# Kernel tuning notes

Hardware: AMD Instinct MI355X
Metric: run time of the kernel (lower is better)

The kernel has to match this reference:

```python
import jax, jax.numpy as jnp
import numpy as np

N_NODES = 100000
N_EDGES = 1600000
D_IN = 264
D_HID = 64
NEG_SLOPE = 0.2


def _glorot(key, shape):
    fan_in, fan_out = shape[0], shape[-1]
    lim = jnp.sqrt(6.0 / (fan_in + fan_out))
    return jax.random.uniform(key, shape, jnp.float32, -lim, lim)


def setup_inputs() -> dict:
    key = jax.random.key(0)
    ks = jax.random.split(key, 24)
    x = jax.random.normal(ks[0], (N_NODES, D_IN), jnp.float32)
    src = jax.random.randint(ks[1], (N_EDGES,), 0, N_NODES, jnp.int32)
    off = jax.random.randint(ks[2], (N_EDGES,), 1, N_NODES, jnp.int32)
    dst = (src + off) % N_NODES  # guaranteed no self loops
    edge_index = jnp.stack([src, dst], axis=0)
    edge_attr = jax.random.normal(ks[3], (N_EDGES, 1), jnp.float32)
    p = {
        'l1_Wl': _glorot(ks[4], (D_IN, D_HID)), 'l1_bl': jnp.zeros((D_HID,), jnp.float32),
        'l1_Wr': _glorot(ks[5], (D_IN, D_HID)), 'l1_br': jnp.zeros((D_HID,), jnp.float32),
        'l1_We': _glorot(ks[6], (1, D_HID)),
        'l1_att': _glorot(ks[7], (1, 1, D_HID)), 'l1_bias': jnp.zeros((D_HID,), jnp.float32),
        'l2_Wl': _glorot(ks[8], (D_HID, D_HID)), 'l2_bl': jnp.zeros((D_HID,), jnp.float32),
        'l2_Wr': _glorot(ks[9], (D_HID, D_HID)), 'l2_br': jnp.zeros((D_HID,), jnp.float32),
        'l2_We': _glorot(ks[10], (1, D_HID)),
        'l2_att': _glorot(ks[11], (1, 1, D_HID)), 'l2_bias': jnp.zeros((D_HID,), jnp.float32),
        'W3': _glorot(ks[12], (D_HID, D_HID)), 'b3': jnp.zeros((D_HID,), jnp.float32),
        'W4': _glorot(ks[13], (D_HID, 1)), 'b4': jnp.zeros((1,), jnp.float32),
    }
    return dict(x=x, edge_index=edge_index, edge_attr=edge_attr, **p)


def _gatv2_layer(x, src, dst, ea, Wl, bl, Wr, br, We, att, bias):
    # heads=1, concat=True, aggr='max' (passed via **kwargs to MessagePassing)
    n = x.shape[0]
    xl = (x @ Wl + bl).reshape(n, 1, D_HID)  # source-side transform
    xr = (x @ Wr + br).reshape(n, 1, D_HID)  # target-side transform
    e = (ea @ We).reshape(-1, 1, D_HID)      # lin_edge, no bias
    m = jax.nn.leaky_relu(xr[dst] + xl[src] + e, NEG_SLOPE)  # (Etot,1,64)
    logits = jnp.sum(m * att, axis=-1)       # (Etot,1)
    # segment softmax over destination nodes
    mx = jax.ops.segment_max(logits, dst, num_segments=n)
    ex = jnp.exp(logits - mx[dst])
    den = jax.ops.segment_sum(ex, dst, num_segments=n)
    alpha = ex / den[dst]                    # (Etot,1)
    msg = xl[src] * alpha[:, :, None]        # (Etot,1,64)
    out = jax.ops.segment_max(msg, dst, num_segments=n)  # aggr='max'
    return out.reshape(n, D_HID) + bias


def _gcn_forward(x, src, dst, edge_attr,
                 l1_Wl, l1_bl, l1_Wr, l1_br, l1_We, l1_att, l1_bias,
                 l2_Wl, l2_bl, l2_Wr, l2_br, l2_We, l2_att, l2_bias,
                 W3, b3, W4, b4):
    n = x.shape[0]
    # add_self_loops with fill_value='mean' (edges contain no self loops)
    loop = jnp.arange(n, dtype=src.dtype)
    src2 = jnp.concatenate([src, loop])
    dst2 = jnp.concatenate([dst, loop])
    mean_ea = jnp.mean(edge_attr, axis=0, keepdims=True)  # (1,1)
    ea2 = jnp.concatenate([edge_attr, jnp.broadcast_to(mean_ea, (n, 1))], axis=0)
    h = _gatv2_layer(x, src2, dst2, ea2, l1_Wl, l1_bl, l1_Wr, l1_br, l1_We, l1_att, l1_bias)
    h = jax.nn.relu(h)  # dropout inactive in eval
    h = _gatv2_layer(h, src2, dst2, ea2, l2_Wl, l2_bl, l2_Wr, l2_br, l2_We, l2_att, l2_bias)
    h = jax.nn.relu(h)
    h = jax.nn.relu(h @ W3 + b3)
    h = h @ W4 + b4
    return jnp.squeeze(h, axis=-1)  # (N,)


def reference(x, edge_index, edge_attr,
              l1_Wl, l1_bl, l1_Wr, l1_br, l1_We, l1_att, l1_bias,
              l2_Wl, l2_bl, l2_Wr, l2_br, l2_We, l2_att, l2_bias,
              W3, b3, W4, b4):
    src, dst = edge_index[0], edge_index[1]
    return _gcn_forward(x, src, dst, edge_attr,
                        l1_Wl, l1_bl, l1_Wr, l1_br, l1_We, l1_att, l1_bias,
                        l2_Wl, l2_bl, l2_Wr, l2_br, l2_We, l2_att, l2_bias,
                        W3, b3, W4, b4)
```

## Files before the change

kernel.cpp:

```cpp
#include <hip/hip_runtime.h>
#include <math.h>
#include <float.h>

#define NN 100000
#define NE 1600000
#define ETOT 1700000
#define DIN 264
#define DH 64
#define SLOPE 0.2f
#define NB 98

__global__ void k_mean(const float* __restrict__ ea, float* __restrict__ sum) {
  float acc = 0.f;
  for (int i = blockIdx.x * blockDim.x + threadIdx.x; i < NE; i += gridDim.x * blockDim.x)
    acc += ea[i];
  #pragma unroll
  for (int off = 32; off > 0; off >>= 1) acc += __shfl_xor(acc, off);
  __shared__ float s[4];
  int lane = threadIdx.x & 63, w = threadIdx.x >> 6;
  if (lane == 0) s[w] = acc;
  __syncthreads();
  if (threadIdx.x == 0) atomicAdd(sum, s[0] + s[1] + s[2] + s[3]);
}

__global__ void k_hist(const int* __restrict__ ei, unsigned* __restrict__ deg) {
  int e = blockIdx.x * blockDim.x + threadIdx.x;
  if (e >= ETOT) return;
  int d = (e < NE) ? ei[NE + e] : e - NE;
  atomicAdd(&deg[d], 1u);
}


__global__ __launch_bounds__(256)
void k_bsum(const unsigned* __restrict__ deg, unsigned* __restrict__ bsum) {
  int i0 = blockIdx.x * 1024 + threadIdx.x * 4;
  unsigned s = 0;
  if (i0 + 3 < NN) {
    uint4 v = *(const uint4*)&deg[i0];
    s = v.x + v.y + v.z + v.w;
  }
  #pragma unroll
  for (int off = 32; off > 0; off >>= 1) s += __shfl_xor(s, off);
  __shared__ unsigned ws[4];
  int lane = threadIdx.x & 63, w = threadIdx.x >> 6;
  if (lane == 0) ws[w] = s;
  __syncthreads();
  if (threadIdx.x == 0) bsum[blockIdx.x] = ws[0] + ws[1] + ws[2] + ws[3];
}

__global__ __launch_bounds__(128)
void k_sscan(unsigned* __restrict__ bsum, unsigned* __restrict__ rowptr) {
  __shared__ unsigned ls[128];
  int t = threadIdx.x;
  unsigned v = (t < NB) ? bsum[t] : 0u;
  ls[t] = v;
  __syncthreads();
  for (int off = 1; off < 128; off <<= 1) {
    unsigned u = (t >= off) ? ls[t - off] : 0u;
    __syncthreads();
    ls[t] += u;
    __syncthreads();
  }
  if (t < NB) bsum[t] = ls[t] - v;
  if (t == 127) rowptr[NN] = ls[127];
}

__global__ __launch_bounds__(256)
void k_scan2(const unsigned* __restrict__ deg, const unsigned* __restrict__ bsum,
             unsigned* __restrict__ rowptr, unsigned* __restrict__ wptr) {
  __shared__ unsigned ls[256];
  int i0 = blockIdx.x * 1024 + threadIdx.x * 4;
  unsigned d0 = 0, d1 = 0, d2 = 0, d3 = 0;
  if (i0 + 3 < NN) {
    uint4 v = *(const uint4*)&deg[i0];
    d0 = v.x; d1 = v.y; d2 = v.z; d3 = v.w;
  }
  unsigned ts = d0 + d1 + d2 + d3;
  ls[threadIdx.x] = ts;
  __syncthreads();
  for (int off = 1; off < 256; off <<= 1) {
    unsigned u = (threadIdx.x >= (unsigned)off) ? ls[threadIdx.x - off] : 0u;
    __syncthreads();
    ls[threadIdx.x] += u;
    __syncthreads();
  }
  unsigned base = bsum[blockIdx.x] + ls[threadIdx.x] - ts;
  if (i0 + 3 < NN) {
    uint4 r;
    r.x = base;
    r.y = base + d0;
    r.z = r.y + d1;
    r.w = r.z + d2;
    *(uint4*)&rowptr[i0] = r;
    *(uint4*)&wptr[i0] = r;
  }
}

__global__ void k_scatter(const int* __restrict__ ei, const float* __restrict__ ea,
                          const float* __restrict__ sump, unsigned* __restrict__ wptr,
                          int2* __restrict__ csr) {
  int e = blockIdx.x * blockDim.x + threadIdx.x;
  if (e >= ETOT) return;
  int s, d;
  float a;
  if (e < NE) {
    s = ei[e];
    d = ei[NE + e];
    a = ea[e];
  } else {
    s = d = e - NE;
    a = sump[0] * (1.0f / NE);
  }
  unsigned pos = atomicAdd(&wptr[d], 1u);
  csr[pos] = make_int2(s, __float_as_int(a));
}

template <int K>
__global__ __launch_bounds__(256)
void k_gemm2(const float* __restrict__ X,
             const float* __restrict__ Wl, const float* __restrict__ bl,
             const float* __restrict__ Wr, const float* __restrict__ br,
             float* __restrict__ xl, float* __restrict__ xr) {
  __shared__ float xs[32 * K];
  const int r0 = blockIdx.x * 32;
  {
    const float* src = X + (size_t)r0 * K;
    for (int i = threadIdx.x * 4; i < 32 * K; i += 256 * 4)
      *(float4*)&xs[i] = *(const float4*)&src[i];
  }
  __syncthreads();
  const int wave = threadIdx.x >> 6;
  const int lane = threadIdx.x & 63;
  const int m0 = wave * 8;
  float accl[8], accr[8];
  #pragma unroll
  for (int m = 0; m < 8; m++) { accl[m] = 0.f; accr[m] = 0.f; }
  for (int kk = 0; kk < K; kk += 4) {
    float wl0 = Wl[(kk + 0) * DH + lane];
    float wl1 = Wl[(kk + 1) * DH + lane];
    float wl2 = Wl[(kk + 2) * DH + lane];
    float wl3 = Wl[(kk + 3) * DH + lane];
    float wr0 = Wr[(kk + 0) * DH + lane];
    float wr1 = Wr[(kk + 1) * DH + lane];
    float wr2 = Wr[(kk + 2) * DH + lane];
    float wr3 = Wr[(kk + 3) * DH + lane];
    #pragma unroll
    for (int m = 0; m < 8; m++) {
      float4 xv = *(const float4*)&xs[(m0 + m) * K + kk];
      accl[m] = fmaf(xv.x, wl0, accl[m]);
      accl[m] = fmaf(xv.y, wl1, accl[m]);
      accl[m] = fmaf(xv.z, wl2, accl[m]);
      accl[m] = fmaf(xv.w, wl3, accl[m]);
      accr[m] = fmaf(xv.x, wr0, accr[m]);
      accr[m] = fmaf(xv.y, wr1, accr[m]);
      accr[m] = fmaf(xv.z, wr2, accr[m]);
      accr[m] = fmaf(xv.w, wr3, accr[m]);
    }
  }
  float blv = bl[lane], brv = br[lane];
  #pragma unroll
  for (int m = 0; m < 8; m++) {
    xl[(r0 + m0 + m) * DH + lane] = accl[m] + blv;
    xr[(r0 + m0 + m) * DH + lane] = accr[m] + brv;
  }
}

template <bool HEAD>
__global__ void k_attn(const unsigned* __restrict__ rowptr, const int2* __restrict__ csr,
                       const float* __restrict__ xl, const float* __restrict__ xr,
                       const float* __restrict__ We, const float* __restrict__ att,
                       const float* __restrict__ bias, float* __restrict__ h,
                       const float* __restrict__ W3, const float* __restrict__ b3,
                       const float* __restrict__ W4, const float* __restrict__ b4,
                       float* __restrict__ out) {
  int n = (blockIdx.x * blockDim.x + threadIdx.x) >> 4;
  int l = threadIdx.x & 15;
  int g0 = threadIdx.x & 48;
  if (n >= NN) return;
  int l4 = l * 4;
  float4 xr4 = *(const float4*)&xr[n * DH + l4];
  float4 we4 = *(const float4*)&We[l4];
  float4 at4 = *(const float4*)&att[l4];
  int beg = rowptr[n], end = rowptr[n + 1];
  float M, D;
  float4 V;
  {
    int2 c0 = csr[beg];
    float a = __int_as_float(c0.y);
    float4 sl = *(const float4*)&xl[c0.x * DH + l4];
    float v, p = 0.f;
    v = xr4.x + sl.x + a * we4.x; v = v > 0.f ? v : SLOPE * v; p += v * at4.x;
    v = xr4.y + sl.y + a * we4.y; v = v > 0.f ? v : SLOPE * v; p += v * at4.y;
    v = xr4.z + sl.z + a * we4.z; v = v > 0.f ? v : SLOPE * v; p += v * at4.z;
    v = xr4.w + sl.w + a * we4.w; v = v > 0.f ? v : SLOPE * v; p += v * at4.w;
    p += __shfl_xor(p, 1);
    p += __shfl_xor(p, 2);
    p += __shfl_xor(p, 4);
    p += __shfl_xor(p, 8);
    M = p; D = 1.f; V = sl;
  }
  for (int e0 = beg + 1; e0 < end; e0 += 16) {
    int2 cl = csr[min(e0 + l, end - 1)];
    int cnt = min(16, end - e0);
    for (int i = 0; i < cnt; i += 4) {
      int mm = min(4, cnt - i);
      float4 sl[4];
      float av[4];
      #pragma unroll
      for (int j = 0; j < 4; j++) {
        if (j < mm) {
          int s = __shfl(cl.x, g0 + i + j);
          av[j] = __int_as_float(__shfl(cl.y, g0 + i + j));
          sl[j] = *(const float4*)&xl[s * DH + l4];
        }
      }
      #pragma unroll
      for (int j = 0; j < 4; j++) {
        if (j < mm) {
          float a = av[j];
          float v, p = 0.f;
          v = xr4.x + sl[j].x + a * we4.x; v = v > 0.f ? v : SLOPE * v; p += v * at4.x;
          v = xr4.y + sl[j].y + a * we4.y; v = v > 0.f ? v : SLOPE * v; p += v * at4.y;
          v = xr4.z + sl[j].z + a * we4.z; v = v > 0.f ? v : SLOPE * v; p += v * at4.z;
          v = xr4.w + sl[j].w + a * we4.w; v = v > 0.f ? v : SLOPE * v; p += v * at4.w;
          p += __shfl_xor(p, 1);
          p += __shfl_xor(p, 2);
          p += __shfl_xor(p, 4);
          p += __shfl_xor(p, 8);
          float Mn = fmaxf(M, p);
          float sO = __expf(M - Mn), sN = __expf(p - Mn);
          D = D * sO + sN;
          V.x = fmaxf(V.x * sO, sl[j].x * sN);
          V.y = fmaxf(V.y * sO, sl[j].y * sN);
          V.z = fmaxf(V.z * sO, sl[j].z * sN);
          V.w = fmaxf(V.w * sO, sl[j].w * sN);
          M = Mn;
        }
      }
    }
  }
  float inv = 1.0f / D;
  float4 b = *(const float4*)&bias[l4];
  float4 o;
  o.x = fmaxf(V.x * inv + b.x, 0.f);
  o.y = fmaxf(V.y * inv + b.y, 0.f);
  o.z = fmaxf(V.z * inv + b.z, 0.f);
  o.w = fmaxf(V.w * inv + b.w, 0.f);
  if (!HEAD) {
    *(float4*)&h[n * DH + l4] = o;
  } else {
    float4 acc = {0.f, 0.f, 0.f, 0.f};
    #pragma unroll
    for (int kk = 0; kk < 16; kk++) {
      float4 hk;
      hk.x = __shfl(o.x, g0 + kk);
      hk.y = __shfl(o.y, g0 + kk);
      hk.z = __shfl(o.z, g0 + kk);
      hk.w = __shfl(o.w, g0 + kk);
      float4 w0 = *(const float4*)&W3[(kk * 4 + 0) * DH + l4];
      acc.x = fmaf(hk.x, w0.x, acc.x);
      acc.y = fmaf(hk.x, w0.y, acc.y);
      acc.z = fmaf(hk.x, w0.z, acc.z);
      acc.w = fmaf(hk.x, w0.w, acc.w);
      float4 w1 = *(const float4*)&W3[(kk * 4 + 1) * DH + l4];
      acc.x = fmaf(hk.y, w1.x, acc.x);
      acc.y = fmaf(hk.y, w1.y, acc.y);
      acc.z = fmaf(hk.y, w1.z, acc.z);
      acc.w = fmaf(hk.y, w1.w, acc.w);
      float4 w2 = *(const float4*)&W3[(kk * 4 + 2) * DH + l4];
      acc.x = fmaf(hk.z, w2.x, acc.x);
      acc.y = fmaf(hk.z, w2.y, acc.y);
      acc.z = fmaf(hk.z, w2.z, acc.z);
      acc.w = fmaf(hk.z, w2.w, acc.w);
      float4 w3 = *(const float4*)&W3[(kk * 4 + 3) * DH + l4];
      acc.x = fmaf(hk.w, w3.x, acc.x);
      acc.y = fmaf(hk.w, w3.y, acc.y);
      acc.z = fmaf(hk.w, w3.z, acc.z);
      acc.w = fmaf(hk.w, w3.w, acc.w);
    }
    float4 b3v = *(const float4*)&b3[l4];
    float4 w4v = *(const float4*)&W4[l4];
    float t, p = 0.f;
    t = acc.x + b3v.x; t = t > 0.f ? t : 0.f; p += t * w4v.x;
    t = acc.y + b3v.y; t = t > 0.f ? t : 0.f; p += t * w4v.y;
    t = acc.z + b3v.z; t = t > 0.f ? t : 0.f; p += t * w4v.z;
    t = acc.w + b3v.w; t = t > 0.f ? t : 0.f; p += t * w4v.w;
    p += __shfl_xor(p, 1);
    p += __shfl_xor(p, 2);
    p += __shfl_xor(p, 4);
    p += __shfl_xor(p, 8);
    if (l == 0) out[n] = p + b4[0];
  }
}

extern "C" void kernel_launch(void* const* d_in, const int* in_sizes, int n_in,
                              void* d_out, int out_size, void* d_ws, size_t ws_size,
                              hipStream_t stream) {
  const float* x      = (const float*)d_in[0];
  const int*   ei     = (const int*)d_in[1];
  const float* ea     = (const float*)d_in[2];
  const float* l1_Wl  = (const float*)d_in[3];
  const float* l1_bl  = (const float*)d_in[4];
  const float* l1_Wr  = (const float*)d_in[5];
  const float* l1_br  = (const float*)d_in[6];
  const float* l1_We  = (const float*)d_in[7];
  const float* l1_att = (const float*)d_in[8];
  const float* l1_bias= (const float*)d_in[9];
  const float* l2_Wl  = (const float*)d_in[10];
  const float* l2_bl  = (const float*)d_in[11];
  const float* l2_Wr  = (const float*)d_in[12];
  const float* l2_br  = (const float*)d_in[13];
  const float* l2_We  = (const float*)d_in[14];
  const float* l2_att = (const float*)d_in[15];
  const float* l2_bias= (const float*)d_in[16];
  const float* W3     = (const float*)d_in[17];
  const float* b3     = (const float*)d_in[18];
  const float* W4     = (const float*)d_in[19];
  const float* b4     = (const float*)d_in[20];
  float* out = (float*)d_out;

  float*    ws     = (float*)d_ws;
  float*    sum    = ws;
  float*    xl     = ws + 256;
  float*    xr     = xl + NN * DH;
  float*    h      = xr + NN * DH;
  int2*     csr    = (int2*)(h + NN * DH);
  unsigned* rowptr = (unsigned*)(csr + ETOT);
  unsigned* wptr   = rowptr + NN + 4;
  unsigned* deg    = wptr + NN;
  unsigned* bsum   = deg + NN;

  const int B = 256;
  const int gemm_blocks = NN / 32;
  const int edge_blocks = (ETOT + B - 1) / B;
  const int attn_blocks = (NN * 16) / B;

  hipMemsetAsync(sum, 0, 256 * sizeof(float), stream);
  hipMemsetAsync(deg, 0, NN * sizeof(unsigned), stream);
  k_mean<<<256, B, 0, stream>>>(ea, sum);
  k_hist<<<edge_blocks, B, 0, stream>>>(ei, deg);
  k_bsum<<<NB, B, 0, stream>>>(deg, bsum);
  k_sscan<<<1, 128, 0, stream>>>(bsum, rowptr);
  k_scan2<<<NB, B, 0, stream>>>(deg, bsum, rowptr, wptr);
  k_scatter<<<edge_blocks, B, 0, stream>>>(ei, ea, sum, wptr, csr);

  k_gemm2<DIN><<<gemm_blocks, B, 0, stream>>>(x, l1_Wl, l1_bl, l1_Wr, l1_br, xl, xr);
  k_attn<false><<<attn_blocks, B, 0, stream>>>(rowptr, csr, xl, xr, l1_We, l1_att,
                                               l1_bias, h, W3, b3, W4, b4, out);

  k_gemm2<DH><<<gemm_blocks, B, 0, stream>>>(h, l2_Wl, l2_bl, l2_Wr, l2_br, xl, xr);
  k_attn<true><<<attn_blocks, B, 0, stream>>>(rowptr, csr, xl, xr, l2_We, l2_att,
                                              l2_bias, h, W3, b3, W4, b4, out);
}
```

Before: 736.2 us.

## Replace FP32 FMA projection GEMMs with split-bf16 MFMA matrix-core GEMMs

The node projection GEMMs (x@Wl, x@Wr for both layers) move from scalar FP32 FMAs to bf16 MFMA instructions. Both operands are split into high and low bf16 parts and three MFMA products are summed, which keeps accuracy close to FP32. A new prep kernel packs the weights into the MFMA fragment layout in workspace, and the GEMM tile grows to 64 rows per block. This trades extra conversion work in shared memory and two small extra launches for much higher matrix throughput, with a small risk of precision differences.

```diff
diff --git a/kernel.cpp b/kernel.cpp
--- a/kernel.cpp
+++ b/kernel.cpp
@@ -9,6 +9,18 @@
 #define DH 64
 #define SLOPE 0.2f
 #define NB 98
+
+typedef __attribute__((ext_vector_type(8))) short s8v;
+typedef __attribute__((ext_vector_type(4))) float f4v;
+
+__device__ __forceinline__ unsigned short f2bf(float x) {
+  unsigned u = __float_as_uint(x);
+  u += 0x7FFFu + ((u >> 16) & 1u);
+  return (unsigned short)(u >> 16);
+}
+__device__ __forceinline__ float bf2f(unsigned short h) {
+  return __uint_as_float(((unsigned)h) << 16);
+}
 
 __global__ void k_mean(const float* __restrict__ ea, float* __restrict__ sum) {
   float acc = 0.f;
@@ -29,7 +41,6 @@
   int d = (e < NE) ? ei[NE + e] : e - NE;
   atomicAdd(&deg[d], 1u);
 }
-
 
 __global__ __launch_bounds__(256)
 void k_bsum(const unsigned* __restrict__ deg, unsigned* __restrict__ bsum) {
@@ -117,51 +128,110 @@
 
 template <int K>
 __global__ __launch_bounds__(256)
-void k_gemm2(const float* __restrict__ X,
-             const float* __restrict__ Wl, const float* __restrict__ bl,
-             const float* __restrict__ Wr, const float* __restrict__ br,
-             float* __restrict__ xl, float* __restrict__ xr) {
-  __shared__ float xs[32 * K];
-  const int r0 = blockIdx.x * 32;
+void k_wprep(const float* __restrict__ Wl, const float* __restrict__ Wr,
+             unsigned short* __restrict__ wfh, unsigned short* __restrict__ wfl) {
+  constexpr int KC = (K + 31) / 32;
+  int t = blockIdx.x * blockDim.x + threadIdx.x;
+  if (t >= 8 * KC * 64) return;
+  int lane = t & 63;
+  int kc = (t >> 6) % KC;
+  int ntg = t / (64 * KC);
+  const float* src = (ntg < 4) ? Wl : Wr;
+  int n = (ntg & 3) * 16 + (lane & 15);
+  int k0 = kc * 32 + (lane >> 4) * 8;
+  #pragma unroll
+  for (int i = 0; i < 8; i++) {
+    int k = k0 + i;
+    float v = (k < K) ? src[k * DH + n] : 0.f;
+    unsigned short hh = f2bf(v);
+    wfh[t * 8 + i] = hh;
+    wfl[t * 8 + i] = f2bf(v - bf2f(hh));
+  }
+}
+
+template <int K>
+__global__ __launch_bounds__(256) __attribute__((amdgpu_waves_per_eu(2)))
+void k_mm(const float* __restrict__ X,
+          const unsigned short* __restrict__ wfh, const unsigned short* __restrict__ wfl,
+          const float* __restrict__ bl, const float* __restrict__ br,
+          float* __restrict__ xl, float* __restrict__ xr) {
+  constexpr int KC = (K + 31) / 32;
+  constexpr int KP = KC * 32;
+  constexpr int SP = KP + 8;
+  __shared__ unsigned short lsh[64 * SP];
+  __shared__ unsigned short lsl[64 * SP];
+  const int r0 = blockIdx.x * 64;
+  const int tid = threadIdx.x;
+  if constexpr (KP > K) {
+    constexpr int PADW = (KP - K) / 2;
+    for (int t = tid; t < 64 * PADW; t += 256) {
+      int row = t / PADW, c = t - row * PADW;
+      *(unsigned*)&lsh[row * SP + K + 2 * c] = 0u;
+      *(unsigned*)&lsl[row * SP + K + 2 * c] = 0u;
+    }
+  }
   {
-    const float* src = X + (size_t)r0 * K;
-    for (int i = threadIdx.x * 4; i < 32 * K; i += 256 * 4)
-      *(float4*)&xs[i] = *(const float4*)&src[i];
+    constexpr int HK = K / 2;
+    for (int p = tid; p < 64 * HK; p += 256) {
+      int row = p / HK, kp = p - row * HK;
+      int grow = r0 + row;
+      float a = 0.f, b = 0.f;
+      if (grow < NN) {
+        float2 v = *(const float2*)&X[(size_t)grow * K + 2 * kp];
+        a = v.x; b = v.y;
+      }
+      unsigned short ha = f2bf(a), hb = f2bf(b);
+      unsigned short la = f2bf(a - bf2f(ha)), lb = f2bf(b - bf2f(hb));
+      *(unsigned*)&lsh[row * SP + 2 * kp] = (unsigned)ha | ((unsigned)hb << 16);
+      *(unsigned*)&lsl[row * SP + 2 * kp] = (unsigned)la | ((unsigned)lb << 16);
+    }
   }
   __syncthreads();
-  const int wave = threadIdx.x >> 6;
-  const int lane = threadIdx.x & 63;
-  const int m0 = wave * 8;
-  float accl[8], accr[8];
+  const int lane = tid & 63, w = tid >> 6;
+  const int kq = lane >> 4;
+  const int ar = lane & 15;
+  f4v acc[4][2];
   #pragma unroll
-  for (int m = 0; m < 8; m++) { accl[m] = 0.f; accr[m] = 0.f; }
-  for (int kk = 0; kk < K; kk += 4) {
-    float wl0 = Wl[(kk + 0) * DH + lane];
-    float wl1 = Wl[(kk + 1) * DH + lane];
-    float wl2 = Wl[(kk + 2) * DH + lane];
-    float wl3 = Wl[(kk + 3) * DH + lane];
-    float wr0 = Wr[(kk + 0) * DH + lane];
-    float wr1 = Wr[(kk + 1) * DH + lane];
-    float wr2 = Wr[(kk + 2) * DH + lane];
-    float wr3 = Wr[(kk + 3) * DH + lane];
+  for (int mt = 0; mt < 4; mt++)
     #pragma unroll
-    for (int m = 0; m < 8; m++) {
-      float4 xv = *(const float4*)&xs[(m0 + m) * K + kk];
-      accl[m] = fmaf(xv.x, wl0, accl[m]);
-      accl[m] = fmaf(xv.y, wl1, accl[m]);
-      accl[m] = fmaf(xv.z, wl2, accl[m]);
-      accl[m] = fmaf(xv.w, wl3, accl[m]);
-      accr[m] = fmaf(xv.x, wr0, accr[m]);
-      accr[m] = fmaf(xv.y, wr1, accr[m]);
-      accr[m] = fmaf(xv.z, wr2, accr[m]);
-      accr[m] = fmaf(xv.w, wr3, accr[m]);
-    }
-  }
-  float blv = bl[lane], brv = br[lane];
+    for (int j = 0; j < 2; j++)
+      acc[mt][j] = (f4v){0.f, 0.f, 0.f, 0.f};
+  for (int kc = 0; kc < KC; kc++) {
+    const int kb = kc * 32 + kq * 8;
+    s8v ah[4], al[4];
+    #pragma unroll
+    for (int mt = 0; mt < 4; mt++) {
+      ah[mt] = *(const s8v*)&lsh[(mt * 16 + ar) * SP + kb];
+      al[mt] = *(const s8v*)&lsl[(mt * 16 + ar) * SP + kb];
+    }
+    #pragma unroll
+    for (int j = 0; j < 2; j++) {
+      const int bidx = (((w * 2 + j) * KC + kc) * 64 + lane) * 8;
+      s8v bh = *(const s8v*)&wfh[bidx];
+      s8v bv = *(const s8v*)&wfl[bidx];
+      #pragma unroll
+      for (int mt = 0; mt < 4; mt++) {
+        acc[mt][j] = __builtin_amdgcn_mfma_f32_16x16x32_bf16(ah[mt], bh, acc[mt][j], 0, 0, 0);
+        acc[mt][j] = __builtin_amdgcn_mfma_f32_16x16x32_bf16(ah[mt], bv, acc[mt][j], 0, 0, 0);
+        acc[mt][j] = __builtin_amdgcn_mfma_f32_16x16x32_bf16(al[mt], bh, acc[mt][j], 0, 0, 0);
+      }
+    }
+  }
+  const int mat = w >> 1;
+  const float* bias = mat ? br : bl;
+  float* outp = mat ? xr : xl;
   #pragma unroll
-  for (int m = 0; m < 8; m++) {
-    xl[(r0 + m0 + m) * DH + lane] = accl[m] + blv;
-    xr[(r0 + m0 + m) * DH + lane] = accr[m] + brv;
+  for (int j = 0; j < 2; j++) {
+    int col = ((w & 1) * 2 + j) * 16 + ar;
+    float bv = bias[col];
+    #pragma unroll
+    for (int mt = 0; mt < 4; mt++) {
+      #pragma unroll
+      for (int r = 0; r < 4; r++) {
+        int grow = r0 + mt * 16 + kq * 4 + r;
+        if (grow < NN) outp[(size_t)grow * DH + col] = acc[mt][j][r] + bv;
+      }
+    }
   }
 }
 
@@ -329,14 +399,20 @@
   unsigned* wptr   = rowptr + NN + 4;
   unsigned* deg    = wptr + NN;
   unsigned* bsum   = deg + NN;
+  unsigned short* wf1h = (unsigned short*)(bsum + 128);
+  unsigned short* wf1l = wf1h + 36864;
+  unsigned short* wf2h = wf1l + 36864;
+  unsigned short* wf2l = wf2h + 8192;
 
   const int B = 256;
-  const int gemm_blocks = NN / 32;
+  const int mm_blocks   = (NN + 63) / 64;
   const int edge_blocks = (ETOT + B - 1) / B;
   const int attn_blocks = (NN * 16) / B;
 
   hipMemsetAsync(sum, 0, 256 * sizeof(float), stream);
   hipMemsetAsync(deg, 0, NN * sizeof(unsigned), stream);
+  k_wprep<DIN><<<(8 * 9 * 64 + B - 1) / B, B, 0, stream>>>(l1_Wl, l1_Wr, wf1h, wf1l);
+  k_wprep<DH><<<(8 * 2 * 64 + B - 1) / B, B, 0, stream>>>(l2_Wl, l2_Wr, wf2h, wf2l);
   k_mean<<<256, B, 0, stream>>>(ea, sum);
   k_hist<<<edge_blocks, B, 0, stream>>>(ei, deg);
   k_bsum<<<NB, B, 0, stream>>>(deg, bsum);
@@ -344,11 +420,11 @@
   k_scan2<<<NB, B, 0, stream>>>(deg, bsum, rowptr, wptr);
   k_scatter<<<edge_blocks, B, 0, stream>>>(ei, ea, sum, wptr, csr);
 
-  k_gemm2<DIN><<<gemm_blocks, B, 0, stream>>>(x, l1_Wl, l1_bl, l1_Wr, l1_br, xl, xr);
+  k_mm<DIN><<<mm_blocks, B, 0, stream>>>(x, wf1h, wf1l, l1_bl, l1_br, xl, xr);
   k_attn<false><<<attn_blocks, B, 0, stream>>>(rowptr, csr, xl, xr, l1_We, l1_att,
                                                l1_bias, h, W3, b3, W4, b4, out);
 
-  k_gemm2<DH><<<gemm_blocks, B, 0, stream>>>(h, l2_Wl, l2_bl, l2_Wr, l2_br, xl, xr);
+  k_mm<DH><<<mm_blocks, B, 0, stream>>>(h, wf2h, wf2l, l2_bl, l2_br, xl, xr);
   k_attn<true><<<attn_blocks, B, 0, stream>>>(rowptr, csr, xl, xr, l2_We, l2_att,
                                               l2_bias, h, W3, b3, W4, b4, out);
 }
```

Result: faster. 710.5 us (-3.5%).
